# Optimization experiments

Measured on AMD Instinct MI355X. Metric: run time of the kernel, lower is better.

The kernel has to match this reference:

```python
import jax, jax.numpy as jnp
import numpy as np

B = 16384
QD = 2048   # query_dim
KD = 1024   # key_dim
HID = 1024  # hidden_dim = min(QD, KD)
NH = 16     # num_heads
HD = HID // NH  # head_dim = 64
LN_EPS = 1e-5


def _ln(x, w, b):
    m = jnp.mean(x, axis=-1, keepdims=True)
    v = jnp.mean((x - m) ** 2, axis=-1, keepdims=True)
    return (x - m) * jax.lax.rsqrt(v + LN_EPS) * w + b


def _lin(x, W, b):
    return x @ W.T + b


def setup_inputs() -> dict:
    key = jax.random.key(0)
    ks = jax.random.split(key, 12)
    p = lambda k, shape: jax.random.normal(k, shape, jnp.float32) * 0.02
    return dict(
        query_features=jax.random.normal(ks[0], (B, QD), jnp.float32),
        key_features=jax.random.normal(ks[1], (B, KD), jnp.float32),
        Wq=p(ks[2], (HID, QD)), bq=jnp.zeros((HID,), jnp.float32),
        ln_q_w=jnp.ones((HID,), jnp.float32), ln_q_b=jnp.zeros((HID,), jnp.float32),
        Wk=p(ks[3], (HID, KD)), bk=jnp.zeros((HID,), jnp.float32),
        ln_k_w=jnp.ones((HID,), jnp.float32), ln_k_b=jnp.zeros((HID,), jnp.float32),
        Wvq=p(ks[4], (HID, QD)), bvq=jnp.zeros((HID,), jnp.float32),
        Wvk=p(ks[5], (HID, KD)), bvk=jnp.zeros((HID,), jnp.float32),
        Wo=p(ks[6], (QD, HID)), bo=jnp.zeros((QD,), jnp.float32),
        ln_o_w=jnp.ones((QD,), jnp.float32), ln_o_b=jnp.zeros((QD,), jnp.float32),
        Wg1=p(ks[7], (HID, QD + KD)), bg1=jnp.zeros((HID,), jnp.float32),
        Wg2=p(ks[8], (1, HID)), bg2=jnp.zeros((1,), jnp.float32),
        Wc1=p(ks[9], (HID, QD + KD)), bc1=jnp.zeros((HID,), jnp.float32),
        Wc2=p(ks[10], (1, HID)), bc2=jnp.zeros((1,), jnp.float32),
    )


def reference(query_features, key_features,
              Wq, bq, ln_q_w, ln_q_b,
              Wk, bk, ln_k_w, ln_k_b,
              Wvq, bvq, Wvk, bvk,
              Wo, bo, ln_o_w, ln_o_b,
              Wg1, bg1, Wg2, bg2,
              Wc1, bc1, Wc2, bc2):
    b = query_features.shape[0]
    q = _ln(_lin(query_features, Wq, bq), ln_q_w, ln_q_b)      # [B, HID]
    k = _ln(_lin(key_features, Wk, bk), ln_k_w, ln_k_b)        # [B, HID]
    v_q = _lin(query_features, Wvq, bvq)  # computed in torch but unused
    v_k = _lin(key_features, Wvk, bvk)    # [B, HID]
    q = q.reshape(b, NH, HD)
    k = k.reshape(b, NH, HD)
    v_k = v_k.reshape(b, NH, HD)
    # NOTE: attention mixes over the HEAD axis (j == num_heads), per original einsum
    scores = jnp.einsum('bhd,bjd->bhj', q, k) / np.sqrt(HD).astype(np.float32)
    attn = jax.nn.softmax(scores, axis=-1)  # dropout p effectively 0 / eval mode
    attended = jnp.einsum('bhj,bjd->bhd', attn, v_k).reshape(b, HID)
    output = _ln(_lin(attended, Wo, bo), ln_o_w, ln_o_b)       # [B, QD]
    combined = jnp.concatenate([query_features, key_features], axis=1)  # [B, QD+KD]
    gate = jax.nn.sigmoid(_lin(jax.nn.gelu(_lin(combined, Wg1, bg1), approximate=False), Wg2, bg2))
    chem = jax.nn.sigmoid(_lin(jax.nn.gelu(_lin(combined, Wc1, bc1), approximate=False), Wc2, bc2))
    effective_gate = gate * chem  # [B, 1]
    return query_features + effective_gate * output
```

## Files before the change

kernel.cpp:

```cpp
#include <hip/hip_runtime.h>
#include <stdint.h>

#define QD 2048
#define KD 1024
#define HID 1024
#define NH 16
#define HD 64
#define CMBD 3072

typedef float  f32x4   __attribute__((ext_vector_type(4)));
typedef short  short8  __attribute__((ext_vector_type(8)));
typedef short  short4v __attribute__((ext_vector_type(4)));
typedef float  float4v __attribute__((ext_vector_type(4)));

__device__ inline float bf2f(short s) {
  unsigned u = ((unsigned)(unsigned short)s) << 16;
  return __builtin_bit_cast(float, u);
}
__device__ inline short f2bf(float f) {
  unsigned u = __builtin_bit_cast(unsigned, f);
  u = u + 0x7fff + ((u >> 16) & 1);
  return (short)(u >> 16);
}

__global__ void cvt_inputs(const float* __restrict__ qf, const float* __restrict__ kf,
                           short* __restrict__ cmb, int rows2) {
  const int b = blockIdx.x, t = threadIdx.x;
  if (b < rows2) {
    const int i = b * 256 + t;
    const int row = i >> 9, c4 = i & 511;
    float4v v = *(const float4v*)(qf + (size_t)row * QD + c4 * 4);
    short4v o;
    o[0] = f2bf(v[0]); o[1] = f2bf(v[1]); o[2] = f2bf(v[2]); o[3] = f2bf(v[3]);
    *(short4v*)(cmb + (size_t)row * CMBD + c4 * 4) = o;
  } else {
    const int i = (b - rows2) * 256 + t;
    const int row = i >> 8, c4 = i & 255;
    float4v v = *(const float4v*)(kf + (size_t)row * KD + c4 * 4);
    short4v o;
    o[0] = f2bf(v[0]); o[1] = f2bf(v[1]); o[2] = f2bf(v[2]); o[3] = f2bf(v[3]);
    *(short4v*)(cmb + (size_t)row * CMBD + QD + c4 * 4) = o;
  }
}

struct WSeg { const float* s; short* d; int blkEnd; };
__global__ void cvt_weights(WSeg s0, WSeg s1, WSeg s2, WSeg s3, WSeg s4, WSeg s5) {
  int b = blockIdx.x;
  WSeg seg; int base;
  if      (b < s0.blkEnd) { seg = s0; base = 0; }
  else if (b < s1.blkEnd) { seg = s1; base = s0.blkEnd; }
  else if (b < s2.blkEnd) { seg = s2; base = s1.blkEnd; }
  else if (b < s3.blkEnd) { seg = s3; base = s2.blkEnd; }
  else if (b < s4.blkEnd) { seg = s4; base = s3.blkEnd; }
  else                    { seg = s5; base = s4.blkEnd; }
  const size_t i = ((size_t)(b - base) * 256 + threadIdx.x) * 4;
  float4v v = *(const float4v*)(seg.s + i);
  short4v o;
  o[0] = f2bf(v[0]); o[1] = f2bf(v[1]); o[2] = f2bf(v[2]); o[3] = f2bf(v[3]);
  *(short4v*)(seg.d + i) = o;
}

__global__ void pack_params(float* __restrict__ egp, int egpN,
                            const float* __restrict__ bg1, const float* __restrict__ bc1,
                            const float* __restrict__ bk,  const float* __restrict__ bvk,
                            const float* __restrict__ Wg2, const float* __restrict__ Wc2,
                            float* __restrict__ bgc, float* __restrict__ bkv,
                            float* __restrict__ w2gc) {
  int i = blockIdx.x * 256 + threadIdx.x;
  if (i < egpN) { egp[i] = 0.f; return; }
  i -= egpN;
  const int seg = i >> 10, idx = i & 1023;
  switch (seg) {
    case 0: bgc[idx]         = bg1[idx]; break;
    case 1: bgc[1024 + idx]  = bc1[idx]; break;
    case 2: bkv[idx]         = bk[idx];  break;
    case 3: bkv[1024 + idx]  = bvk[idx]; break;
    case 4: w2gc[idx]        = Wg2[idx]; break;
    case 5: w2gc[1024 + idx] = Wc2[idx]; break;
  }
}

#define EPI_NONE 0
#define EPI_GATE 2

typedef const __attribute__((address_space(1))) void gvoid_t;
typedef __attribute__((address_space(3))) void lvoid_t;

#define WAIT_VM(n)  asm volatile("s_waitcnt vmcnt(" #n ")" ::: "memory")

#define APAN(b, kp) (((b) * 2 + (kp)) * 8192)
#define BPAN(b, kp) (32768 + ((b) * 2 + (kp)) * 8192)

#define PHASE_MID                                        \
  __builtin_amdgcn_s_barrier();                          \
  asm volatile("s_waitcnt lgkmcnt(0)" ::: "memory");     \
  __builtin_amdgcn_s_setprio(1);

#define PHASE_END                                        \
  __builtin_amdgcn_s_setprio(0);                         \
  __builtin_amdgcn_s_barrier();

template<int EPI>
__global__ __launch_bounds__(512, 2)
void gemm256(const short* __restrict__ A, size_t lda,
             const short* __restrict__ W,
             const float* __restrict__ bias,
             short* __restrict__ C, int N, int K,
             const float* __restrict__ w2, float* __restrict__ egp, int rowsTot) {
  extern __shared__ short ls[];
  const int tid  = threadIdx.x;
  const int lane = tid & 63;
  const int wave = tid >> 6;
  const int wm = wave >> 2, wn = wave & 3;
  const int fr = lane & 15, kq4 = lane >> 4;

  const int nwg = gridDim.x * gridDim.y;
  const int lin = blockIdx.y * gridDim.x + blockIdx.x;
  const int cpx = nwg >> 3;
  const int nid = (lin & 7) * cpx + (lin >> 3);
  const int bx = nid % gridDim.x, by = nid / gridDim.x;
  const size_t rowBase = (size_t)by * 256;
  const size_t colBase = (size_t)bx * 256;

  const int NTT = K >> 6;

  f32x4 acc[8][4];
#pragma unroll
  for (int mi = 0; mi < 8; mi++)
#pragma unroll
    for (int ni = 0; ni < 4; ni++) acc[mi][ni] = (f32x4){0.f, 0.f, 0.f, 0.f};

  const int frsw = (kq4 ^ ((fr >> 1) & 3)) * 8;

  const int grow  = tid >> 2;
  const int slotx = (tid & 3) ^ ((tid >> 3) & 3);
  const short* gAlo = A + (rowBase + grow) * lda + slotx * 8;
  const short* gAhi = gAlo + (size_t)128 * lda;
  const short* gBlo = W + (colBase + grow) * (size_t)K + slotx * 8;
  const short* gBhi = gBlo + (size_t)128 * K;
  short* const sdst = ls + tid * 8;

  auto STG_A = [&](int panOff, int kcol) {
    __builtin_amdgcn_global_load_lds((gvoid_t*)(gAlo + kcol), (lvoid_t*)(sdst + panOff),        16, 0, 0);
    __builtin_amdgcn_global_load_lds((gvoid_t*)(gAhi + kcol), (lvoid_t*)(sdst + panOff + 4096), 16, 0, 0);
  };
  auto STG_B = [&](int panOff, int kcol) {
    __builtin_amdgcn_global_load_lds((gvoid_t*)(gBlo + kcol), (lvoid_t*)(sdst + panOff),        16, 0, 0);
    __builtin_amdgcn_global_load_lds((gvoid_t*)(gBhi + kcol), (lvoid_t*)(sdst + panOff + 4096), 16, 0, 0);
  };

  STG_A(APAN(0, 0), 0);  STG_A(APAN(0, 1), 32);
  STG_B(BPAN(0, 0), 0);  STG_B(BPAN(0, 1), 32);
  STG_B(BPAN(1, 0), 64); STG_B(BPAN(1, 1), 96);
  WAIT_VM(4);
  __builtin_amdgcn_s_barrier();

  short8 fa0[8], fa1[8], fb0[4], fb1[4];

  for (int t = 0; t < NTT; t += 2) {
    const bool more = (t + 2 < NTT);
    const int kA1 = (t + 1) * 64;
    const int kE2 = (t + 2) * 64;
    const int kO3 = (t + 3) * 64;

#pragma unroll
    for (int m = 0; m < 4; m++) {
      const int r = (wm * 128 + m * 16 + fr) * 32 + frsw;
      fa0[m * 2 + 0] = *(const short8*)(ls + APAN(0, 0) + r);
      fa0[m * 2 + 1] = *(const short8*)(ls + APAN(0, 1) + r);
    }
#pragma unroll
    for (int n = 0; n < 2; n++) {
      const int r = (wn * 64 + n * 16 + fr) * 32 + frsw;
      fb0[n * 2 + 0] = *(const short8*)(ls + BPAN(0, 0) + r);
      fb0[n * 2 + 1] = *(const short8*)(ls + BPAN(0, 1) + r);
    }
    STG_A(APAN(1, 0), kA1);
    PHASE_MID
#pragma unroll
    for (int m = 0; m < 4; m++)
#pragma unroll
      for (int n = 0; n < 2; n++) {
        acc[m][n] = __builtin_amdgcn_mfma_f32_16x16x32_bf16(fa0[m*2+0], fb0[n*2+0], acc[m][n], 0, 0, 0);
        acc[m][n] = __builtin_amdgcn_mfma_f32_16x16x32_bf16(fa0[m*2+1], fb0[n*2+1], acc[m][n], 0, 0, 0);
      }
    PHASE_END

#pragma unroll
    for (int n = 0; n < 2; n++) {
      const int r = (wn * 64 + (n + 2) * 16 + fr) * 32 + frsw;
      fb1[n * 2 + 0] = *(const short8*)(ls + BPAN(0, 0) + r);
      fb1[n * 2 + 1] = *(const short8*)(ls + BPAN(0, 1) + r);
    }
    STG_A(APAN(1, 1), kA1 + 32);
    PHASE_MID
#pragma unroll
    for (int m = 0; m < 4; m++)
#pragma unroll
      for (int n = 0; n < 2; n++) {
        acc[m][n+2] = __builtin_amdgcn_mfma_f32_16x16x32_bf16(fa0[m*2+0], fb1[n*2+0], acc[m][n+2], 0, 0, 0);
        acc[m][n+2] = __builtin_amdgcn_mfma_f32_16x16x32_bf16(fa0[m*2+1], fb1[n*2+1], acc[m][n+2], 0, 0, 0);
      }
    PHASE_END

#pragma unroll
    for (int m = 0; m < 4; m++) {
      const int r = (wm * 128 + (m + 4) * 16 + fr) * 32 + frsw;
      fa1[m * 2 + 0] = *(const short8*)(ls + APAN(0, 0) + r);
      fa1[m * 2 + 1] = *(const short8*)(ls + APAN(0, 1) + r);
    }
    if (more) STG_B(BPAN(0, 0), kE2);
    PHASE_MID
#pragma unroll
    for (int m = 0; m < 4; m++)
#pragma unroll
      for (int n = 0; n < 2; n++) {
        acc[m+4][n] = __builtin_amdgcn_mfma_f32_16x16x32_bf16(fa1[m*2+0], fb0[n*2+0], acc[m+4][n], 0, 0, 0);
        acc[m+4][n] = __builtin_amdgcn_mfma_f32_16x16x32_bf16(fa1[m*2+1], fb0[n*2+1], acc[m+4][n], 0, 0, 0);
      }
    PHASE_END

    if (more) STG_B(BPAN(0, 1), kE2 + 32);
    PHASE_MID
#pragma unroll
    for (int m = 0; m < 4; m++)
#pragma unroll
      for (int n = 0; n < 2; n++) {
        acc[m+4][n+2] = __builtin_amdgcn_mfma_f32_16x16x32_bf16(fa1[m*2+0], fb1[n*2+0], acc[m+4][n+2], 0, 0, 0);
        acc[m+4][n+2] = __builtin_amdgcn_mfma_f32_16x16x32_bf16(fa1[m*2+1], fb1[n*2+1], acc[m+4][n+2], 0, 0, 0);
      }
    __builtin_amdgcn_s_setprio(0);
    if (more) { WAIT_VM(4); } else { WAIT_VM(0); }
    __builtin_amdgcn_s_barrier();

#pragma unroll
    for (int m = 0; m < 4; m++) {
      const int r = (wm * 128 + m * 16 + fr) * 32 + frsw;
      fa0[m * 2 + 0] = *(const short8*)(ls + APAN(1, 0) + r);
      fa0[m * 2 + 1] = *(const short8*)(ls + APAN(1, 1) + r);
    }
#pragma unroll
    for (int n = 0; n < 2; n++) {
      const int r = (wn * 64 + n * 16 + fr) * 32 + frsw;
      fb0[n * 2 + 0] = *(const short8*)(ls + BPAN(1, 0) + r);
      fb0[n * 2 + 1] = *(const short8*)(ls + BPAN(1, 1) + r);
    }
    if (more) STG_A(APAN(0, 0), kE2);
    PHASE_MID
#pragma unroll
    for (int m = 0; m < 4; m++)
#pragma unroll
      for (int n = 0; n < 2; n++) {
        acc[m][n] = __builtin_amdgcn_mfma_f32_16x16x32_bf16(fa0[m*2+0], fb0[n*2+0], acc[m][n], 0, 0, 0);
        acc[m][n] = __builtin_amdgcn_mfma_f32_16x16x32_bf16(fa0[m*2+1], fb0[n*2+1], acc[m][n], 0, 0, 0);
      }
    PHASE_END

#pragma unroll
    for (int n = 0; n < 2; n++) {
      const int r = (wn * 64 + (n + 2) * 16 + fr) * 32 + frsw;
      fb1[n * 2 + 0] = *(const short8*)(ls + BPAN(1, 0) + r);
      fb1[n * 2 + 1] = *(const short8*)(ls + BPAN(1, 1) + r);
    }
    if (more) STG_A(APAN(0, 1), kE2 + 32);
    PHASE_MID
#pragma unroll
    for (int m = 0; m < 4; m++)
#pragma unroll
      for (int n = 0; n < 2; n++) {
        acc[m][n+2] = __builtin_amdgcn_mfma_f32_16x16x32_bf16(fa0[m*2+0], fb1[n*2+0], acc[m][n+2], 0, 0, 0);
        acc[m][n+2] = __builtin_amdgcn_mfma_f32_16x16x32_bf16(fa0[m*2+1], fb1[n*2+1], acc[m][n+2], 0, 0, 0);
      }
    PHASE_END

#pragma unroll
    for (int m = 0; m < 4; m++) {
      const int r = (wm * 128 + (m + 4) * 16 + fr) * 32 + frsw;
      fa1[m * 2 + 0] = *(const short8*)(ls + APAN(1, 0) + r);
      fa1[m * 2 + 1] = *(const short8*)(ls + APAN(1, 1) + r);
    }
    if (more) STG_B(BPAN(1, 0), kO3);
    PHASE_MID
#pragma unroll
    for (int m = 0; m < 4; m++)
#pragma unroll
      for (int n = 0; n < 2; n++) {
        acc[m+4][n] = __builtin_amdgcn_mfma_f32_16x16x32_bf16(fa1[m*2+0], fb0[n*2+0], acc[m+4][n], 0, 0, 0);
        acc[m+4][n] = __builtin_amdgcn_mfma_f32_16x16x32_bf16(fa1[m*2+1], fb0[n*2+1], acc[m+4][n], 0, 0, 0);
      }
    PHASE_END

    if (more) STG_B(BPAN(1, 1), kO3 + 32);
    PHASE_MID
#pragma unroll
    for (int m = 0; m < 4; m++)
#pragma unroll
      for (int n = 0; n < 2; n++) {
        acc[m+4][n+2] = __builtin_amdgcn_mfma_f32_16x16x32_bf16(fa1[m*2+0], fb1[n*2+0], acc[m+4][n+2], 0, 0, 0);
        acc[m+4][n+2] = __builtin_amdgcn_mfma_f32_16x16x32_bf16(fa1[m*2+1], fb1[n*2+1], acc[m+4][n+2], 0, 0, 0);
      }
    __builtin_amdgcn_s_setprio(0);
    if (more) { WAIT_VM(4); }
    __builtin_amdgcn_s_barrier();
  }

  if (EPI == EPI_GATE) {
    float w2v[4], bvv[4];
#pragma unroll
    for (int ni = 0; ni < 4; ni++) {
      const int c = (int)colBase + wn * 64 + ni * 16 + fr;
      w2v[ni] = w2[c]; bvv[ni] = bias[c];
    }
    const int half = (colBase >= 1024) ? 1 : 0;
#pragma unroll
    for (int mi = 0; mi < 8; mi++) {
      float sj[4] = {0.f, 0.f, 0.f, 0.f};
#pragma unroll
      for (int ni = 0; ni < 4; ni++)
#pragma unroll
        for (int j = 0; j < 4; j++) {
          float x = acc[mi][ni][j] + bvv[ni];
          float g = 0.5f * x * (1.f + erff(x * 0.70710678118f));
          sj[j] += g * w2v[ni];
        }
#pragma unroll
      for (int j = 0; j < 4; j++) {
#pragma unroll
        for (int o = 8; o >= 1; o >>= 1) sj[j] += __shfl_xor(sj[j], o);
        if (fr == 0) {
          const int row = (int)rowBase + wm * 128 + mi * 16 + kq4 * 4 + j;
          atomicAdd(egp + half * rowsTot + row, sj[j]);
        }
      }
    }
  } else {
#pragma unroll
    for (int mi = 0; mi < 8; mi++) {
      const size_t row0 = rowBase + wm * 128 + mi * 16 + kq4 * 4;
#pragma unroll
      for (int ni = 0; ni < 4; ni++) {
        const int col = (int)colBase + wn * 64 + ni * 16 + fr;
        const float bv = bias[col];
#pragma unroll
        for (int j = 0; j < 4; j++) {
          float x = acc[mi][ni][j] + bv;
          C[(row0 + j) * (size_t)N + col] = f2bf(x);
        }
      }
    }
  }
}

__device__ inline float4 block_sum4(float a, float b, float c, float d, float* sc) {
#pragma unroll
  for (int o = 32; o >= 1; o >>= 1) {
    a += __shfl_down(a, o); b += __shfl_down(b, o);
    c += __shfl_down(c, o); d += __shfl_down(d, o);
  }
  const int lane = threadIdx.x & 63, w = threadIdx.x >> 6;
  const int nw = blockDim.x >> 6;
  if (lane == 0) { sc[w*4] = a; sc[w*4+1] = b; sc[w*4+2] = c; sc[w*4+3] = d; }
  __syncthreads();
  float ra = 0.f, rb = 0.f, rc = 0.f, rd = 0.f;
  for (int i = 0; i < nw; i++) { ra += sc[i*4]; rb += sc[i*4+1]; rc += sc[i*4+2]; rd += sc[i*4+3]; }
  __syncthreads();
  return make_float4(ra, rb, rc, rd);
}
__device__ inline float2 block_sum2(float a, float b, float* sc) {
#pragma unroll
  for (int o = 32; o >= 1; o >>= 1) { a += __shfl_down(a, o); b += __shfl_down(b, o); }
  const int lane = threadIdx.x & 63, w = threadIdx.x >> 6;
  const int nw = blockDim.x >> 6;
  if (lane == 0) { sc[w*2] = a; sc[w*2+1] = b; }
  __syncthreads();
  float ra = 0.f, rb = 0.f;
  for (int i = 0; i < nw; i++) { ra += sc[i*2]; rb += sc[i*2+1]; }
  __syncthreads();
  return make_float2(ra, rb);
}

__global__ __launch_bounds__(256)
void attn_ln(const short* __restrict__ qp, const short* __restrict__ kv,
             const float* __restrict__ lnqw, const float* __restrict__ lnqb,
             const float* __restrict__ lnkw, const float* __restrict__ lnkb,
             short* __restrict__ att) {
  __shared__ float qs[HID];
  __shared__ float ks[NH * 65];
  __shared__ float vs[HID];
  __shared__ float aw[256];
  __shared__ float red[16];
  const int t = threadIdx.x;
  const size_t row = blockIdx.x;

  short4v q4 = *(const short4v*)(qp + row * HID + t * 4);
  short4v k4 = *(const short4v*)(kv + row * 2048 + t * 4);
  short4v v4 = *(const short4v*)(kv + row * 2048 + 1024 + t * 4);
  float qv[4], kvv[4];
  float sq = 0.f, sqq = 0.f, sk = 0.f, skk = 0.f;
#pragma unroll
  for (int i = 0; i < 4; i++) {
    qv[i] = bf2f(q4[i]); sq += qv[i]; sqq += qv[i] * qv[i];
    kvv[i] = bf2f(k4[i]); sk += kvv[i]; skk += kvv[i] * kvv[i];
  }
  float4 r4 = block_sum4(sq, sqq, sk, skk, red);
  float mq = r4.x / HID, vq = r4.y / HID - mq * mq;
  float rsq = rsqrtf(vq + 1e-5f);
  float mk = r4.z / HID, vv = r4.w / HID - mk * mk;
  float rsk = rsqrtf(vv + 1e-5f);
#pragma unroll
  for (int i = 0; i < 4; i++) {
    const int idx = t * 4 + i;
    qs[idx] = (qv[i] - mq) * rsq * lnqw[idx] + lnqb[idx];
    ks[(idx >> 6) * 65 + (idx & 63)] = (kvv[i] - mk) * rsk * lnkw[idx] + lnkb[idx];
    vs[idx] = bf2f(v4[i]);
  }
  __syncthreads();

  const int h = t >> 4, j = t & 15;
  float s = 0.f;
#pragma unroll 8
  for (int d = 0; d < 64; d++) s += qs[h * 64 + d] * ks[j * 65 + d];
  s *= 0.125f;
  float mx = s;
#pragma unroll
  for (int o = 8; o >= 1; o >>= 1) mx = fmaxf(mx, __shfl_xor(mx, o, 16));
  float e = __expf(s - mx);
  float sum = e;
#pragma unroll
  for (int o = 8; o >= 1; o >>= 1) sum += __shfl_xor(sum, o, 16);
  aw[t] = e / sum;
  __syncthreads();

  const int dB = (t & 15) * 4;
  float o0 = 0.f, o1 = 0.f, o2 = 0.f, o3 = 0.f;
#pragma unroll
  for (int jj = 0; jj < 16; jj++) {
    const float w = aw[h * 16 + jj];
    const float* vp = &vs[jj * 64 + dB];
    o0 += w * vp[0]; o1 += w * vp[1]; o2 += w * vp[2]; o3 += w * vp[3];
  }
  short4v o4;
  o4[0] = f2bf(o0); o4[1] = f2bf(o1); o4[2] = f2bf(o2); o4[3] = f2bf(o3);
  *(short4v*)(att + row * HID + h * 64 + dB) = o4;
}

__global__ __launch_bounds__(256)
void final_kernel(const short* __restrict__ opre, const short* __restrict__ cmb,
                  const float* __restrict__ egp, int rowsTot,
                  const float* __restrict__ bg2, const float* __restrict__ bc2,
                  const float* __restrict__ lnow, const float* __restrict__ lnob,
                  float* __restrict__ out) {
  __shared__ float red[8];
  const int t = threadIdx.x;
  const size_t row = blockIdx.x;
  short8 o8 = *(const short8*)(opre + row * QD + t * 8);
  short8 q8 = *(const short8*)(cmb + row * CMBD + t * 8);
  float x[8];
  float s = 0.f, ss = 0.f;
#pragma unroll
  for (int i = 0; i < 8; i++) { x[i] = bf2f(o8[i]); s += x[i]; ss += x[i] * x[i]; }
  float2 r = block_sum2(s, ss, red);
  float m = r.x / QD, v = r.y / QD - m * m;
  float rs = rsqrtf(v + 1e-5f);
  float gg = 1.f / (1.f + __expf(-(egp[row] + bg2[0])));
  float gc = 1.f / (1.f + __expf(-(egp[rowsTot + row] + bc2[0])));
  float g = gg * gc;
  float4v oa, ob;
#pragma unroll
  for (int i = 0; i < 8; i++) {
    const int c = t * 8 + i;
    float y = (x[i] - m) * rs * lnow[c] + lnob[c];
    float r2 = bf2f(q8[i]) + g * y;
    if (i < 4) oa[i] = r2; else ob[i - 4] = r2;
  }
  *(float4v*)(out + row * QD + t * 8) = oa;
  *(float4v*)(out + row * QD + t * 8 + 4) = ob;
}

extern "C" void kernel_launch(void* const* d_in, const int* in_sizes, int n_in,
                              void* d_out, int out_size, void* d_ws, size_t ws_size,
                              hipStream_t stream) {
  const float* qf   = (const float*)d_in[0];
  const float* kf   = (const float*)d_in[1];
  const float* Wq   = (const float*)d_in[2];
  const float* bq   = (const float*)d_in[3];
  const float* lnqw = (const float*)d_in[4];
  const float* lnqb = (const float*)d_in[5];
  const float* Wk   = (const float*)d_in[6];
  const float* bk   = (const float*)d_in[7];
  const float* lnkw = (const float*)d_in[8];
  const float* lnkb = (const float*)d_in[9];
  const float* Wvk  = (const float*)d_in[12];
  const float* bvk  = (const float*)d_in[13];
  const float* Wo   = (const float*)d_in[14];
  const float* bo   = (const float*)d_in[15];
  const float* lnow = (const float*)d_in[16];
  const float* lnob = (const float*)d_in[17];
  const float* Wg1  = (const float*)d_in[18];
  const float* bg1  = (const float*)d_in[19];
  const float* Wg2  = (const float*)d_in[20];
  const float* bg2  = (const float*)d_in[21];
  const float* Wc1  = (const float*)d_in[22];
  const float* bc1  = (const float*)d_in[23];
  const float* Wc2  = (const float*)d_in[24];
  const float* bc2  = (const float*)d_in[25];

  const int rows = in_sizes[0] / QD;

  char* ws = (char*)d_ws;
  size_t off = 0;
  auto alloc = [&](size_t bytes) -> char* {
    char* p = ws + off;
    off += (bytes + 255) & ~(size_t)255;
    return p;
  };
  short* cmb  = (short*)alloc((size_t)rows * CMBD * 2);
  short* wqb  = (short*)alloc((size_t)HID * QD * 2);
  short* wkv  = (short*)alloc((size_t)2 * HID * KD * 2);
  short* wob  = (short*)alloc((size_t)QD * HID * 2);
  short* wgc  = (short*)alloc((size_t)2 * HID * CMBD * 2);
  short* hgc  = (short*)alloc((size_t)rows * 2048 * 2);
  short* qp   = (short*)alloc((size_t)rows * HID * 2);
  short* kvp  = (short*)alloc((size_t)rows * 2048 * 2);
  float* egp  = (float*)alloc((size_t)2 * rows * 4);
  float* bgc  = (float*)alloc(2048 * 4);
  float* bkv  = (float*)alloc(2048 * 4);
  float* w2gc = (float*)alloc(2048 * 4);
  short* att  = hgc;
  short* opre = kvp;

  const int egpN = 2 * rows;
  pack_params<<<(egpN + 6144) / 256, 256, 0, stream>>>(egp, egpN, bg1, bc1, bk, bvk,
                                                       Wg2, Wc2, bgc, bkv, w2gc);

  cvt_inputs<<<rows * 3, 256, 0, stream>>>(qf, kf, cmb, rows * 2);
  {
    WSeg s0{Wq,  wqb,                       2048};
    WSeg s1{Wk,  wkv,                       2048 + 1024};
    WSeg s2{Wvk, wkv + (size_t)HID * KD,    2048 + 2048};
    WSeg s3{Wo,  wob,                       2048 + 2048 + 2048};
    WSeg s4{Wg1, wgc,                       2048 + 2048 + 2048 + 3072};
    WSeg s5{Wc1, wgc + (size_t)HID * CMBD,  2048 + 2048 + 2048 + 3072 + 3072};
    cvt_weights<<<s5.blkEnd, 256, 0, stream>>>(s0, s1, s2, s3, s4, s5);
  }

  hipFuncSetAttribute((const void*)gemm256<EPI_GATE>,
                      hipFuncAttributeMaxDynamicSharedMemorySize, 131072);
  hipFuncSetAttribute((const void*)gemm256<EPI_NONE>,
                      hipFuncAttributeMaxDynamicSharedMemorySize, 131072);

  const dim3 blk(512);
  const int mt = rows / 256;
  const size_t lds = 131072;

  gemm256<EPI_GATE><<<dim3(2048 / 256, mt), blk, lds, stream>>>(cmb, CMBD, wgc, bgc, hgc, 2048, CMBD, w2gc, egp, rows);
  gemm256<EPI_NONE><<<dim3(1024 / 256, mt), blk, lds, stream>>>(cmb, CMBD, wqb, bq, qp, 1024, QD, nullptr, nullptr, 0);
  gemm256<EPI_NONE><<<dim3(2048 / 256, mt), blk, lds, stream>>>(cmb + QD, CMBD, wkv, bkv, kvp, 2048, KD, nullptr, nullptr, 0);
  attn_ln<<<rows, 256, 0, stream>>>(qp, kvp, lnqw, lnqb, lnkw, lnkb, att);
  gemm256<EPI_NONE><<<dim3(2048 / 256, mt), blk, lds, stream>>>(att, HID, wob, bo, opre, 2048, HID, nullptr, nullptr, 0);
  final_kernel<<<rows, 256, 0, stream>>>(opre, cmb, egp, rows, bg2, bc2, lnow, lnob, (float*)d_out);
}
```

Baseline: 590.6 us.

## Run gate/chem GEMM in FP8 with a dedicated fp8 MFMA kernel

Adds FP8 (e4m3) conversion of the combined inputs and the Wg1/Wc1 weights, plus a new gemm_gate8 kernel that uses fp8 MFMA instructions with 64 KB of static LDS and two workgroups per CU. The gate/chem GEMM, the largest in the pipeline, is meant to get double MFMA throughput and half the operand bandwidth. In exchange, input conversion writes an extra fp8 copy using a slow software converter, and accuracy drops for the gate values, which could exceed the tolerance.

```diff
diff --git a/kernel.cpp b/kernel.cpp
--- a/kernel.cpp
+++ b/kernel.cpp
@@ -22,42 +22,68 @@
   u = u + 0x7fff + ((u >> 16) & 1);
   return (short)(u >> 16);
 }
+__device__ inline unsigned char f2f8(float f) {
+  unsigned u = __builtin_bit_cast(unsigned, f);
+  unsigned s = (u >> 24) & 0x80u;
+  float a = fabsf(f);
+  if (a >= 448.f) return (unsigned char)(s | 0x7E);
+  if (a < 0.015625f) {
+    int m = (int)(a * 512.f + 0.5f);
+    if (m > 7) return (unsigned char)(s | 0x08);
+    return (unsigned char)(s | m);
+  }
+  int ebits = (int)((u >> 23) & 0xFF) - 127;
+  unsigned mant = u & 0x7FFFFF;
+  unsigned keep = mant >> 20;
+  unsigned rest = mant & 0xFFFFF;
+  keep += (rest > 0x80000u) || (rest == 0x80000u && (keep & 1));
+  if (keep == 8) { keep = 0; ebits += 1; }
+  if (ebits > 8) return (unsigned char)(s | 0x7E);
+  return (unsigned char)(s | ((unsigned)(ebits + 7) << 3) | keep);
+}
 
 __global__ void cvt_inputs(const float* __restrict__ qf, const float* __restrict__ kf,
-                           short* __restrict__ cmb, int rows2) {
+                           short* __restrict__ cmb, unsigned char* __restrict__ cmb8,
+                           int rows2) {
   const int b = blockIdx.x, t = threadIdx.x;
-  if (b < rows2) {
-    const int i = b * 256 + t;
-    const int row = i >> 9, c4 = i & 511;
-    float4v v = *(const float4v*)(qf + (size_t)row * QD + c4 * 4);
-    short4v o;
-    o[0] = f2bf(v[0]); o[1] = f2bf(v[1]); o[2] = f2bf(v[2]); o[3] = f2bf(v[3]);
-    *(short4v*)(cmb + (size_t)row * CMBD + c4 * 4) = o;
-  } else {
-    const int i = (b - rows2) * 256 + t;
-    const int row = i >> 8, c4 = i & 255;
-    float4v v = *(const float4v*)(kf + (size_t)row * KD + c4 * 4);
-    short4v o;
-    o[0] = f2bf(v[0]); o[1] = f2bf(v[1]); o[2] = f2bf(v[2]); o[3] = f2bf(v[3]);
-    *(short4v*)(cmb + (size_t)row * CMBD + QD + c4 * 4) = o;
-  }
+  int row, c4, base;
+  const float* src;
+  if (b < rows2) { const int i = b * 256 + t; row = i >> 9; c4 = i & 511; base = 0;  src = qf + (size_t)row * QD + c4 * 4; }
+  else           { const int i = (b - rows2) * 256 + t; row = i >> 8; c4 = i & 255; base = QD; src = kf + (size_t)row * KD + c4 * 4; }
+  float4v v = *(const float4v*)src;
+  short4v o;
+  o[0] = f2bf(v[0]); o[1] = f2bf(v[1]); o[2] = f2bf(v[2]); o[3] = f2bf(v[3]);
+  *(short4v*)(cmb + (size_t)row * CMBD + base + c4 * 4) = o;
+  unsigned p = (unsigned)f2f8(v[0]) | ((unsigned)f2f8(v[1]) << 8) |
+               ((unsigned)f2f8(v[2]) << 16) | ((unsigned)f2f8(v[3]) << 24);
+  *(unsigned*)(cmb8 + (size_t)row * CMBD + base + c4 * 4) = p;
 }
 
 struct WSeg { const float* s; short* d; int blkEnd; };
-__global__ void cvt_weights(WSeg s0, WSeg s1, WSeg s2, WSeg s3, WSeg s4, WSeg s5) {
+__global__ void cvt_weights(WSeg s0, WSeg s1, WSeg s2, WSeg s3) {
   int b = blockIdx.x;
   WSeg seg; int base;
   if      (b < s0.blkEnd) { seg = s0; base = 0; }
   else if (b < s1.blkEnd) { seg = s1; base = s0.blkEnd; }
   else if (b < s2.blkEnd) { seg = s2; base = s1.blkEnd; }
-  else if (b < s3.blkEnd) { seg = s3; base = s2.blkEnd; }
-  else if (b < s4.blkEnd) { seg = s4; base = s3.blkEnd; }
-  else                    { seg = s5; base = s4.blkEnd; }
+  else                    { seg = s3; base = s2.blkEnd; }
   const size_t i = ((size_t)(b - base) * 256 + threadIdx.x) * 4;
   float4v v = *(const float4v*)(seg.s + i);
   short4v o;
   o[0] = f2bf(v[0]); o[1] = f2bf(v[1]); o[2] = f2bf(v[2]); o[3] = f2bf(v[3]);
   *(short4v*)(seg.d + i) = o;
+}
+
+__global__ void cvt_w8(const float* __restrict__ Wg1, const float* __restrict__ Wc1,
+                       unsigned char* __restrict__ wgc8, int half) {
+  const int b = blockIdx.x;
+  const float* s = (b < half) ? Wg1 : Wc1;
+  unsigned char* d = wgc8 + (b < half ? 0 : (size_t)HID * CMBD);
+  const size_t i = ((size_t)(b < half ? b : b - half) * 256 + threadIdx.x) * 4;
+  float4v v = *(const float4v*)(s + i);
+  unsigned p = (unsigned)f2f8(v[0]) | ((unsigned)f2f8(v[1]) << 8) |
+               ((unsigned)f2f8(v[2]) << 16) | ((unsigned)f2f8(v[3]) << 24);
+  *(unsigned*)(d + i) = p;
 }
 
 __global__ void pack_params(float* __restrict__ egp, int egpN,
@@ -304,48 +330,247 @@
     __builtin_amdgcn_s_barrier();
   }
 
-  if (EPI == EPI_GATE) {
-    float w2v[4], bvv[4];
+#pragma unroll
+  for (int mi = 0; mi < 8; mi++) {
+    const size_t row0 = rowBase + wm * 128 + mi * 16 + kq4 * 4;
 #pragma unroll
     for (int ni = 0; ni < 4; ni++) {
-      const int c = (int)colBase + wn * 64 + ni * 16 + fr;
-      w2v[ni] = w2[c]; bvv[ni] = bias[c];
-    }
-    const int half = (colBase >= 1024) ? 1 : 0;
-#pragma unroll
-    for (int mi = 0; mi < 8; mi++) {
-      float sj[4] = {0.f, 0.f, 0.f, 0.f};
-#pragma unroll
-      for (int ni = 0; ni < 4; ni++)
-#pragma unroll
-        for (int j = 0; j < 4; j++) {
-          float x = acc[mi][ni][j] + bvv[ni];
-          float g = 0.5f * x * (1.f + erff(x * 0.70710678118f));
-          sj[j] += g * w2v[ni];
-        }
+      const int col = (int)colBase + wn * 64 + ni * 16 + fr;
+      const float bv = bias[col];
 #pragma unroll
       for (int j = 0; j < 4; j++) {
-#pragma unroll
-        for (int o = 8; o >= 1; o >>= 1) sj[j] += __shfl_xor(sj[j], o);
-        if (fr == 0) {
-          const int row = (int)rowBase + wm * 128 + mi * 16 + kq4 * 4 + j;
-          atomicAdd(egp + half * rowsTot + row, sj[j]);
-        }
-      }
-    }
-  } else {
-#pragma unroll
-    for (int mi = 0; mi < 8; mi++) {
-      const size_t row0 = rowBase + wm * 128 + mi * 16 + kq4 * 4;
-#pragma unroll
-      for (int ni = 0; ni < 4; ni++) {
-        const int col = (int)colBase + wn * 64 + ni * 16 + fr;
-        const float bv = bias[col];
-#pragma unroll
-        for (int j = 0; j < 4; j++) {
-          float x = acc[mi][ni][j] + bv;
-          C[(row0 + j) * (size_t)N + col] = f2bf(x);
-        }
+        float x = acc[mi][ni][j] + bv;
+        C[(row0 + j) * (size_t)N + col] = f2bf(x);
+      }
+    }
+  }
+}
+
+__global__ __launch_bounds__(512, 2)
+void gemm_gate8(const unsigned char* __restrict__ A,
+                const unsigned char* __restrict__ W,
+                const float* __restrict__ bias,
+                const float* __restrict__ w2, float* __restrict__ egp, int rowsTot) {
+  __shared__ unsigned char ls[65536];
+  const int tid  = threadIdx.x;
+  const int lane = tid & 63;
+  const int wave = tid >> 6;
+  const int wm = wave >> 2, wn = wave & 3;
+  const int fr = lane & 15, kq4 = lane >> 4;
+
+  const int nwg = gridDim.x * gridDim.y;
+  const int lin = blockIdx.y * gridDim.x + blockIdx.x;
+  const int cpx = nwg >> 3;
+  const int nid = (lin & 7) * cpx + (lin >> 3);
+  const int bx = nid % gridDim.x, by = nid / gridDim.x;
+  const size_t rowBase = (size_t)by * 256;
+  const size_t colBase = (size_t)bx * 256;
+
+  const int NTT = CMBD >> 6;
+
+  f32x4 acc[8][4];
+#pragma unroll
+  for (int mi = 0; mi < 8; mi++)
+#pragma unroll
+    for (int ni = 0; ni < 4; ni++) acc[mi][ni] = (f32x4){0.f, 0.f, 0.f, 0.f};
+
+  const int g16 = (((kq4 >> 1) ^ ((fr >> 2) & 1)) << 4) + (kq4 & 1) * 8;
+  const int aoff = (wm * 128 + fr) * 32 + g16;
+  const int boff = 32768 + (wn * 64 + fr) * 32 + g16;
+
+  const int srow = tid >> 1;
+  const int sg   = (tid & 1) ^ ((tid >> 3) & 1);
+  const unsigned char* gA = A + (rowBase + srow) * (size_t)CMBD + sg * 16;
+  const unsigned char* gB = W + (colBase + srow) * (size_t)CMBD + sg * 16;
+  unsigned char* const sdst = ls + tid * 16;
+
+  auto STG_A = [&](int panOff, int kcol) {
+    __builtin_amdgcn_global_load_lds((gvoid_t*)(gA + kcol), (lvoid_t*)(sdst + panOff), 16, 0, 0);
+  };
+  auto STG_B = [&](int panOff, int kcol) {
+    __builtin_amdgcn_global_load_lds((gvoid_t*)(gB + kcol), (lvoid_t*)(sdst + panOff + 32768), 16, 0, 0);
+  };
+
+  STG_A(APAN(0, 0), 0);  STG_A(APAN(0, 1), 32);
+  STG_B(APAN(0, 0), 0);  STG_B(APAN(0, 1), 32);
+  STG_B(APAN(1, 0), 64); STG_B(APAN(1, 1), 96);
+  WAIT_VM(2);
+  __builtin_amdgcn_s_barrier();
+
+  long long fa0[8], fa1[8], fb0[4], fb1[4];
+
+  for (int t = 0; t < NTT; t += 2) {
+    const bool more = (t + 2 < NTT);
+    const int kA1 = (t + 1) * 64;
+    const int kE2 = (t + 2) * 64;
+    const int kO3 = (t + 3) * 64;
+
+#pragma unroll
+    for (int m = 0; m < 4; m++) {
+      const int r = aoff + m * 512;
+      fa0[m * 2 + 0] = *(const long long*)(ls + APAN(0, 0) + r);
+      fa0[m * 2 + 1] = *(const long long*)(ls + APAN(0, 1) + r);
+    }
+#pragma unroll
+    for (int n = 0; n < 2; n++) {
+      const int r = boff + n * 512;
+      fb0[n * 2 + 0] = *(const long long*)(ls + APAN(0, 0) + r);
+      fb0[n * 2 + 1] = *(const long long*)(ls + APAN(0, 1) + r);
+    }
+    STG_A(APAN(1, 0), kA1);
+    PHASE_MID
+#pragma unroll
+    for (int m = 0; m < 4; m++)
+#pragma unroll
+      for (int n = 0; n < 2; n++) {
+        acc[m][n] = __builtin_amdgcn_mfma_f32_16x16x32_fp8_fp8(fa0[m*2+0], fb0[n*2+0], acc[m][n], 0, 0, 0);
+        acc[m][n] = __builtin_amdgcn_mfma_f32_16x16x32_fp8_fp8(fa0[m*2+1], fb0[n*2+1], acc[m][n], 0, 0, 0);
+      }
+    PHASE_END
+
+#pragma unroll
+    for (int n = 0; n < 2; n++) {
+      const int r = boff + (n + 2) * 512;
+      fb1[n * 2 + 0] = *(const long long*)(ls + APAN(0, 0) + r);
+      fb1[n * 2 + 1] = *(const long long*)(ls + APAN(0, 1) + r);
+    }
+    STG_A(APAN(1, 1), kA1 + 32);
+    PHASE_MID
+#pragma unroll
+    for (int m = 0; m < 4; m++)
+#pragma unroll
+      for (int n = 0; n < 2; n++) {
+        acc[m][n+2] = __builtin_amdgcn_mfma_f32_16x16x32_fp8_fp8(fa0[m*2+0], fb1[n*2+0], acc[m][n+2], 0, 0, 0);
+        acc[m][n+2] = __builtin_amdgcn_mfma_f32_16x16x32_fp8_fp8(fa0[m*2+1], fb1[n*2+1], acc[m][n+2], 0, 0, 0);
+      }
+    PHASE_END
+
+#pragma unroll
+    for (int m = 0; m < 4; m++) {
+      const int r = aoff + (m + 4) * 512;
+      fa1[m * 2 + 0] = *(const long long*)(ls + APAN(0, 0) + r);
+      fa1[m * 2 + 1] = *(const long long*)(ls + APAN(0, 1) + r);
+    }
+    if (more) STG_B(APAN(0, 0), kE2);
+    PHASE_MID
+#pragma unroll
+    for (int m = 0; m < 4; m++)
+#pragma unroll
+      for (int n = 0; n < 2; n++) {
+        acc[m+4][n] = __builtin_amdgcn_mfma_f32_16x16x32_fp8_fp8(fa1[m*2+0], fb0[n*2+0], acc[m+4][n], 0, 0, 0);
+        acc[m+4][n] = __builtin_amdgcn_mfma_f32_16x16x32_fp8_fp8(fa1[m*2+1], fb0[n*2+1], acc[m+4][n], 0, 0, 0);
+      }
+    PHASE_END
+
+    if (more) STG_B(APAN(0, 1), kE2 + 32);
+    PHASE_MID
+#pragma unroll
+    for (int m = 0; m < 4; m++)
+#pragma unroll
+      for (int n = 0; n < 2; n++) {
+        acc[m+4][n+2] = __builtin_amdgcn_mfma_f32_16x16x32_fp8_fp8(fa1[m*2+0], fb1[n*2+0], acc[m+4][n+2], 0, 0, 0);
+        acc[m+4][n+2] = __builtin_amdgcn_mfma_f32_16x16x32_fp8_fp8(fa1[m*2+1], fb1[n*2+1], acc[m+4][n+2], 0, 0, 0);
+      }
+    __builtin_amdgcn_s_setprio(0);
+    if (more) { WAIT_VM(2); } else { WAIT_VM(0); }
+    __builtin_amdgcn_s_barrier();
+
+#pragma unroll
+    for (int m = 0; m < 4; m++) {
+      const int r = aoff + m * 512;
+      fa0[m * 2 + 0] = *(const long long*)(ls + APAN(1, 0) + r);
+      fa0[m * 2 + 1] = *(const long long*)(ls + APAN(1, 1) + r);
+    }
+#pragma unroll
+    for (int n = 0; n < 2; n++) {
+      const int r = boff + n * 512;
+      fb0[n * 2 + 0] = *(const long long*)(ls + APAN(1, 0) + r);
+      fb0[n * 2 + 1] = *(const long long*)(ls + APAN(1, 1) + r);
+    }
+    if (more) STG_A(APAN(0, 0), kE2);
+    PHASE_MID
+#pragma unroll
+    for (int m = 0; m < 4; m++)
+#pragma unroll
+      for (int n = 0; n < 2; n++) {
+        acc[m][n] = __builtin_amdgcn_mfma_f32_16x16x32_fp8_fp8(fa0[m*2+0], fb0[n*2+0], acc[m][n], 0, 0, 0);
+        acc[m][n] = __builtin_amdgcn_mfma_f32_16x16x32_fp8_fp8(fa0[m*2+1], fb0[n*2+1], acc[m][n], 0, 0, 0);
+      }
+    PHASE_END
+
+#pragma unroll
+    for (int n = 0; n < 2; n++) {
+      const int r = boff + (n + 2) * 512;
+      fb1[n * 2 + 0] = *(const long long*)(ls + APAN(1, 0) + r);
+      fb1[n * 2 + 1] = *(const long long*)(ls + APAN(1, 1) + r);
+    }
+    if (more) STG_A(APAN(0, 1), kE2 + 32);
+    PHASE_MID
+#pragma unroll
+    for (int m = 0; m < 4; m++)
+#pragma unroll
+      for (int n = 0; n < 2; n++) {
+        acc[m][n+2] = __builtin_amdgcn_mfma_f32_16x16x32_fp8_fp8(fa0[m*2+0], fb1[n*2+0], acc[m][n+2], 0, 0, 0);
+        acc[m][n+2] = __builtin_amdgcn_mfma_f32_16x16x32_fp8_fp8(fa0[m*2+1], fb1[n*2+1], acc[m][n+2], 0, 0, 0);
+      }
+    PHASE_END
+
+#pragma unroll
+    for (int m = 0; m < 4; m++) {
+      const int r = aoff + (m + 4) * 512;
+      fa1[m * 2 + 0] = *(const long long*)(ls + APAN(1, 0) + r);
+      fa1[m * 2 + 1] = *(const long long*)(ls + APAN(1, 1) + r);
+    }
+    if (more) STG_B(APAN(1, 0), kO3);
+    PHASE_MID
+#pragma unroll
+    for (int m = 0; m < 4; m++)
+#pragma unroll
+      for (int n = 0; n < 2; n++) {
+        acc[m+4][n] = __builtin_amdgcn_mfma_f32_16x16x32_fp8_fp8(fa1[m*2+0], fb0[n*2+0], acc[m+4][n], 0, 0, 0);
+        acc[m+4][n] = __builtin_amdgcn_mfma_f32_16x16x32_fp8_fp8(fa1[m*2+1], fb0[n*2+1], acc[m+4][n], 0, 0, 0);
+      }
+    PHASE_END
+
+    if (more) STG_B(APAN(1, 1), kO3 + 32);
+    PHASE_MID
+#pragma unroll
+    for (int m = 0; m < 4; m++)
+#pragma unroll
+      for (int n = 0; n < 2; n++) {
+        acc[m+4][n+2] = __builtin_amdgcn_mfma_f32_16x16x32_fp8_fp8(fa1[m*2+0], fb1[n*2+0], acc[m+4][n+2], 0, 0, 0);
+        acc[m+4][n+2] = __builtin_amdgcn_mfma_f32_16x16x32_fp8_fp8(fa1[m*2+1], fb1[n*2+1], acc[m+4][n+2], 0, 0, 0);
+      }
+    __builtin_amdgcn_s_setprio(0);
+    if (more) { WAIT_VM(2); }
+    __builtin_amdgcn_s_barrier();
+  }
+
+  float w2v[4], bvv[4];
+#pragma unroll
+  for (int ni = 0; ni < 4; ni++) {
+    const int c = (int)colBase + wn * 64 + ni * 16 + fr;
+    w2v[ni] = w2[c]; bvv[ni] = bias[c];
+  }
+  const int half = (colBase >= 1024) ? 1 : 0;
+#pragma unroll
+  for (int mi = 0; mi < 8; mi++) {
+    float sj[4] = {0.f, 0.f, 0.f, 0.f};
+#pragma unroll
+    for (int ni = 0; ni < 4; ni++)
+#pragma unroll
+      for (int j = 0; j < 4; j++) {
+        float x = acc[mi][ni][j] + bvv[ni];
+        float g = 0.5f * x * (1.f + erff(x * 0.70710678118f));
+        sj[j] += g * w2v[ni];
+      }
+#pragma unroll
+    for (int j = 0; j < 4; j++) {
+#pragma unroll
+      for (int o = 8; o >= 1; o >>= 1) sj[j] += __shfl_xor(sj[j], o);
+      if (fr == 0) {
+        const int row = (int)rowBase + wm * 128 + mi * 16 + kq4 * 4 + j;
+        atomicAdd(egp + half * rowsTot + row, sj[j]);
       }
     }
   }
@@ -518,7 +743,7 @@
   short* wqb  = (short*)alloc((size_t)HID * QD * 2);
   short* wkv  = (short*)alloc((size_t)2 * HID * KD * 2);
   short* wob  = (short*)alloc((size_t)QD * HID * 2);
-  short* wgc  = (short*)alloc((size_t)2 * HID * CMBD * 2);
+  unsigned char* wgc8 = (unsigned char*)alloc((size_t)2 * HID * CMBD);
   short* hgc  = (short*)alloc((size_t)rows * 2048 * 2);
   short* qp   = (short*)alloc((size_t)rows * HID * 2);
   short* kvp  = (short*)alloc((size_t)rows * 2048 * 2);
@@ -527,25 +752,23 @@
   float* bkv  = (float*)alloc(2048 * 4);
   float* w2gc = (float*)alloc(2048 * 4);
   short* att  = hgc;
+  unsigned char* cmb8 = (unsigned char*)hgc;
   short* opre = kvp;
 
   const int egpN = 2 * rows;
   pack_params<<<(egpN + 6144) / 256, 256, 0, stream>>>(egp, egpN, bg1, bc1, bk, bvk,
                                                        Wg2, Wc2, bgc, bkv, w2gc);
 
-  cvt_inputs<<<rows * 3, 256, 0, stream>>>(qf, kf, cmb, rows * 2);
+  cvt_inputs<<<rows * 3, 256, 0, stream>>>(qf, kf, cmb, cmb8, rows * 2);
   {
-    WSeg s0{Wq,  wqb,                       2048};
-    WSeg s1{Wk,  wkv,                       2048 + 1024};
-    WSeg s2{Wvk, wkv + (size_t)HID * KD,    2048 + 2048};
-    WSeg s3{Wo,  wob,                       2048 + 2048 + 2048};
-    WSeg s4{Wg1, wgc,                       2048 + 2048 + 2048 + 3072};
-    WSeg s5{Wc1, wgc + (size_t)HID * CMBD,  2048 + 2048 + 2048 + 3072 + 3072};
-    cvt_weights<<<s5.blkEnd, 256, 0, stream>>>(s0, s1, s2, s3, s4, s5);
-  }
-
-  hipFuncSetAttribute((const void*)gemm256<EPI_GATE>,
-                      hipFuncAttributeMaxDynamicSharedMemorySize, 131072);
+    WSeg s0{Wq,  wqb,                    2048};
+    WSeg s1{Wk,  wkv,                    2048 + 1024};
+    WSeg s2{Wvk, wkv + (size_t)HID * KD, 2048 + 2048};
+    WSeg s3{Wo,  wob,                    2048 + 2048 + 2048};
+    cvt_weights<<<s3.blkEnd, 256, 0, stream>>>(s0, s1, s2, s3);
+  }
+  cvt_w8<<<6144, 256, 0, stream>>>(Wg1, Wc1, wgc8, 3072);
+
   hipFuncSetAttribute((const void*)gemm256<EPI_NONE>,
                       hipFuncAttributeMaxDynamicSharedMemorySize, 131072);
 
@@ -553,7 +776,7 @@
   const int mt = rows / 256;
   const size_t lds = 131072;
 
-  gemm256<EPI_GATE><<<dim3(2048 / 256, mt), blk, lds, stream>>>(cmb, CMBD, wgc, bgc, hgc, 2048, CMBD, w2gc, egp, rows);
+  gemm_gate8<<<dim3(8, mt), blk, 0, stream>>>(cmb8, wgc8, bgc, w2gc, egp, rows);
   gemm256<EPI_NONE><<<dim3(1024 / 256, mt), blk, lds, stream>>>(cmb, CMBD, wqb, bq, qp, 1024, QD, nullptr, nullptr, 0);
   gemm256<EPI_NONE><<<dim3(2048 / 256, mt), blk, lds, stream>>>(cmb + QD, CMBD, wkv, bkv, kvp, 2048, KD, nullptr, nullptr, 0);
   attn_ln<<<rows, 256, 0, stream>>>(qp, kvp, lnqw, lnqb, lnkw, lnkb, att);
```

Measured after the change: 591.3 us. No clear change (+0.1%).
